# Performance work log

Hardware: AMD Instinct MI355X
Metric: run time of the kernel (lower is better)

## Reference

```python
import jax, jax.numpy as jnp
import numpy as np
import math

B, L, D = 4, 1024, 1024
H, S = 16, 64
HD = D // H
EPS_LN = 1e-12


def _band_logits_init():
    bl = np.zeros((H, S), dtype=np.float32)
    for h in range(H):
        center = (h + 0.5) * (S / max(H, 1.0))
        for s in range(S):
            dist = s + 0.5 - center
            bl[h, s] = -dist * dist
    return jnp.asarray(bl)


def setup_inputs() -> dict:
    key = jax.random.key(0)
    ks = jax.random.split(key, 12)
    std = 1.0 / math.sqrt(D)
    inp = {
        "hidden_states": jax.random.normal(ks[0], (B, L, D), jnp.float32),
        "attention_mask": jnp.zeros((B, 1, 1, L), jnp.float32),
        "cos_phi": jax.random.normal(ks[1], (B, S, L), jnp.float32),
        "sin_phi": jax.random.normal(ks[2], (B, S, L), jnp.float32),
        "mag": jax.random.uniform(ks[3], (B, S, L), jnp.float32),
        "Wq": jax.random.normal(ks[4], (D, D), jnp.float32) * std,
        "bq": jnp.zeros((D,), jnp.float32),
        "Wk": jax.random.normal(ks[5], (D, D), jnp.float32) * std,
        "bk": jnp.zeros((D,), jnp.float32),
        "Wv": jax.random.normal(ks[6], (D, D), jnp.float32) * std,
        "bv": jnp.zeros((D,), jnp.float32),
        "Wo": jax.random.normal(ks[7], (D, D), jnp.float32) * std,
        "bo": jnp.zeros((D,), jnp.float32),
        "band_logits": _band_logits_init(),
        "phase_bias": jnp.full((H,), 0.5, jnp.float32),
        "gamma": jnp.full((H, S), -3.0, jnp.float32),
        "ln_w": jnp.ones((D,), jnp.float32),
        "ln_b": jnp.zeros((D,), jnp.float32),
    }
    return inp


def _shape_heads(x):
    # [B,L,D] -> [B,H,L,HD]
    return x.reshape(B, L, H, HD).transpose(0, 2, 1, 3)


def reference(hidden_states, attention_mask, cos_phi, sin_phi, mag,
              Wq, bq, Wk, bk, Wv, bv, Wo, bo,
              band_logits, phase_bias, gamma, ln_w, ln_b):
    residual = hidden_states
    q = _shape_heads(hidden_states @ Wq.T + bq)
    k = _shape_heads(hidden_states @ Wk.T + bk)
    v = _shape_heads(hidden_states @ Wv.T + bv)

    cos_pl = cos_phi.transpose(0, 2, 1)  # [B,L,S]
    sin_pl = sin_phi.transpose(0, 2, 1)
    mag_pl = mag.transpose(0, 2, 1)
    mag_pl = mag_pl / (mag_pl.mean(axis=-1, keepdims=True) + 1e-8)

    gamma_pos = jax.nn.softplus(gamma)  # [H,S]
    mag_mix = jnp.tanh(jnp.einsum('bls,hs->bhl', mag_pl, gamma_pos))
    scale = 1.0 + 0.5 * mag_mix[..., None]  # [B,H,L,1]
    q = q * scale
    k = k * scale
    v = v * scale

    attn_scores = jnp.einsum('bhld,bhmd->bhlm', q, k) / math.sqrt(HD)

    band_w_sqrt = jnp.sqrt(jax.nn.softmax(band_logits, axis=-1) + 1e-8)  # [H,S]
    cos_feat = cos_pl[:, None] * band_w_sqrt[None, :, None, :]  # [B,H,L,S]
    sin_feat = sin_pl[:, None] * band_w_sqrt[None, :, None, :]
    phase_align = (jnp.einsum('bhls,bhms->bhlm', cos_feat, cos_feat)
                   + jnp.einsum('bhls,bhms->bhlm', sin_feat, sin_feat)) / math.sqrt(S)

    phase_scale = jax.nn.softplus(phase_bias)[None, :, None, None]
    attn_scores = attn_scores + phase_scale * phase_align + attention_mask

    attn_probs = jax.nn.softmax(attn_scores, axis=-1)
    context = jnp.einsum('bhlm,bhmd->bhld', attn_probs, v)
    context = context.transpose(0, 2, 1, 3).reshape(B, L, D)

    out = context @ Wo.T + bo
    x = out + residual
    mu = x.mean(axis=-1, keepdims=True)
    var = ((x - mu) ** 2).mean(axis=-1, keepdims=True)
    return (x - mu) / jnp.sqrt(var + EPS_LN) * ln_w + ln_b
```

## Files before the change

kernel.cpp:

```cpp
#include <hip/hip_runtime.h>
#include <hip/hip_bf16.h>
#include <math.h>

#define DEV __device__ __forceinline__

typedef __attribute__((ext_vector_type(8))) short short8;
typedef __attribute__((ext_vector_type(8))) unsigned short ushort8v;
typedef __attribute__((ext_vector_type(4))) float f32x4;

DEV unsigned short f2bf(float f) {
  unsigned u = __float_as_uint(f);
  u = u + 0x7fffu + ((u >> 16) & 1u);
  return (unsigned short)(u >> 16);
}

DEV float softplus_f(float x) {
  return (x > 20.f) ? x : log1pf(expf(x));
}

DEV int sw64(int r, int e) { return r * 64 + (e ^ (((r) & 7) << 3)); }
DEV int sw128(int r, int e) { return r * 128 + (e ^ (((r) & 7) << 3)); }

#define GL16(gp, lp) __builtin_amdgcn_global_load_lds( \
    (const __attribute__((address_space(1))) unsigned int*)(gp), \
    (__attribute__((address_space(3))) unsigned int*)(lp), 16, 0, 0)

__global__ __launch_bounds__(256) void k_convall(
    const float* __restrict__ hs, const float* __restrict__ wq,
    const float* __restrict__ wk, const float* __restrict__ wv,
    const float* __restrict__ wo, ushort4* __restrict__ hsb4,
    ushort4* __restrict__ wcat4, ushort4* __restrict__ wob4) {
  const int i = blockIdx.x * 256 + threadIdx.x;
  const float* src;
  ushort4* dst;
  int off;
  if (i < 1048576) {
    src = hs; dst = hsb4; off = i;
  } else {
    const int j = i - 1048576;
    const int g = j >> 18;
    off = j & 262143;
    if (g == 0)      { src = wq; dst = wcat4; }
    else if (g == 1) { src = wk; dst = wcat4 + 262144; }
    else if (g == 2) { src = wv; dst = wcat4 + 524288; }
    else             { src = wo; dst = wob4; }
  }
  const float4 v = reinterpret_cast<const float4*>(src)[off];
  ushort4 o;
  o.x = f2bf(v.x); o.y = f2bf(v.y); o.z = f2bf(v.z); o.w = f2bf(v.w);
  dst[off] = o;
}

__global__ __launch_bounds__(256) void k_prep(
    const float* __restrict__ cos_phi, const float* __restrict__ sin_phi,
    const float* __restrict__ mag, const float* __restrict__ band_logits,
    const float* __restrict__ phase_bias, const float* __restrict__ gamma,
    float* __restrict__ scaleB, unsigned short* __restrict__ feat) {
  const int b = blockIdx.x >> 6;
  const int l0 = ((blockIdx.x >> 2) & 15) << 6;
  const int hq = blockIdx.x & 3;
  const int t = threadIdx.x, lane = t & 63, w = t >> 6;
  __shared__ float cosL[64][65];
  __shared__ float sinL[64][65];
  __shared__ float magL[64][65];
  __shared__ float psum[4][64];
  __shared__ float minv[64];
  __shared__ float bwssL[4][64];
  __shared__ float gposL[4][64];

  {
    const int h = (hq << 2) + w;
    float bl = band_logits[h * 64 + lane];
    float mx = bl;
#pragma unroll
    for (int m = 1; m < 64; m <<= 1) mx = fmaxf(mx, __shfl_xor(mx, m));
    float e = __expf(bl - mx);
    float sm = e;
#pragma unroll
    for (int m = 1; m < 64; m <<= 1) sm += __shfl_xor(sm, m);
    const float ps = softplus_f(phase_bias[h]);
    bwssL[w][lane] = sqrtf(e / sm + 1e-8f) * sqrtf(ps * 0.125f);
    gposL[w][lane] = softplus_f(gamma[h * 64 + lane]);
  }

  const size_t boff = (size_t)b * 65536;
  for (int it = 0; it < 16; ++it) {
    const int s = it * 4 + w, l = lane;
    const size_t g = boff + (size_t)s * 1024 + l0 + l;
    cosL[s][l] = cos_phi[g];
    sinL[s][l] = sin_phi[g];
    magL[s][l] = mag[g];
  }
  __syncthreads();
  {
    const int l = t & 63, g = t >> 6;
    float acc = 0.f;
    for (int i = 0; i < 16; ++i) acc += magL[g * 16 + i][l];
    psum[g][l] = acc;
  }
  __syncthreads();
  if (t < 64) {
    float mean = (psum[0][t] + psum[1][t] + psum[2][t] + psum[3][t]) * (1.f / 64.f);
    minv[t] = 1.f / (mean + 1e-8f);
  }
  __syncthreads();
  {
    const int l = lane;
    const float iv = minv[l];
    const int hidx = (hq << 2) + w;
    float acc = 0.f;
    for (int s = 0; s < 64; ++s) acc += magL[s][l] * gposL[w][s];
    const float tnh = tanhf(acc * iv);
    scaleB[(size_t)(((b << 4) + hidx) << 10) + l0 + l] = 1.f + 0.5f * tnh;
  }
  const int l = t >> 2, sq = (t & 3) << 4;
  for (int hh = 0; hh < 4; ++hh) {
    const int h = (hq << 2) + hh;
    unsigned short* fp = feat + ((size_t)(((b << 4) + h) << 10) + l0 + l) * 128;
    unsigned short cb[16], sb[16];
#pragma unroll
    for (int j = 0; j < 16; ++j) {
      const int s = sq + j;
      const float bw = bwssL[hh][s];
      cb[j] = f2bf(bw * cosL[s][l]);
      sb[j] = f2bf(bw * sinL[s][l]);
    }
    *reinterpret_cast<ushort8v*>(fp + sq) = *reinterpret_cast<ushort8v*>(cb);
    *reinterpret_cast<ushort8v*>(fp + sq + 8) = *reinterpret_cast<ushort8v*>(cb + 8);
    *reinterpret_cast<ushort8v*>(fp + 64 + sq) = *reinterpret_cast<ushort8v*>(sb);
    *reinterpret_cast<ushort8v*>(fp + 64 + sq + 8) = *reinterpret_cast<ushort8v*>(sb + 8);
  }
}

template <int MODE>
__global__ __launch_bounds__(256) void k_gemm(
    const unsigned short* __restrict__ A, const unsigned short* __restrict__ Bt,
    int Ntiles, int K,
    const float* __restrict__ bq, const float* __restrict__ bk,
    const float* __restrict__ bv, const float* __restrict__ scaleB,
    unsigned short* __restrict__ qbuf, unsigned short* __restrict__ kbuf,
    unsigned short* __restrict__ vT,
    const float* __restrict__ bo, const float* __restrict__ resid,
    float* __restrict__ xout) {
  __shared__ __align__(16) short As[128 * 64];
  __shared__ __align__(16) short Bs[128 * 64];
  const int t = threadIdx.x;
  const int lane = t & 63;
  const int w = t >> 6;
  const int cpx = gridDim.x >> 3;
  const int swz = (blockIdx.x & 7) * cpx + (blockIdx.x >> 3);
  const int tm = (swz / Ntiles) << 7;
  const int tn = (swz % Ntiles) << 7;
  const int wR = (w >> 1) << 6;
  const int wC = (w & 1) << 6;
  const int rowS = t >> 3;
  const int offS = (t & 7) << 3;
  const int sgm = (rowS & 7) << 3;
  const int ka = (lane >> 4) << 3;
  const int lm = lane & 15;

  const f32x4 vzero = {0.f, 0.f, 0.f, 0.f};
  f32x4 acc[4][4];
#pragma unroll
  for (int i = 0; i < 4; ++i)
#pragma unroll
    for (int j = 0; j < 4; ++j) acc[i][j] = vzero;

  for (int kt = 0; kt < K; kt += 64) {
    __syncthreads();
#pragma unroll
    for (int p = 0; p < 4; ++p) {
      GL16(A + (size_t)(tm + p * 32 + rowS) * K + kt + (offS ^ sgm), (char*)As + p * 4096 + w * 1024);
      GL16(Bt + (size_t)(tn + p * 32 + rowS) * K + kt + (offS ^ sgm), (char*)Bs + p * 4096 + w * 1024);
    }
    __syncthreads();
    short8 af[4][2], bf[4][2];
#pragma unroll
    for (int mt = 0; mt < 4; ++mt) {
      const int r = wR + mt * 16 + lm;
      af[mt][0] = *(const short8*)&As[sw64(r, ka)];
      af[mt][1] = *(const short8*)&As[sw64(r, 32 + ka)];
    }
#pragma unroll
    for (int nt = 0; nt < 4; ++nt) {
      const int r = wC + nt * 16 + lm;
      bf[nt][0] = *(const short8*)&Bs[sw64(r, ka)];
      bf[nt][1] = *(const short8*)&Bs[sw64(r, 32 + ka)];
    }
#pragma unroll
    for (int mt = 0; mt < 4; ++mt)
#pragma unroll
      for (int nt = 0; nt < 4; ++nt) {
        acc[mt][nt] = __builtin_amdgcn_mfma_f32_16x16x32_bf16(af[mt][0], bf[nt][0], acc[mt][nt], 0, 0, 0);
        acc[mt][nt] = __builtin_amdgcn_mfma_f32_16x16x32_bf16(af[mt][1], bf[nt][1], acc[mt][nt], 0, 0, 0);
      }
  }

#pragma unroll
  for (int mt = 0; mt < 4; ++mt) {
#pragma unroll
    for (int r = 0; r < 4; ++r) {
      const int row = tm + wR + mt * 16 + ((lane >> 4) << 2) + r;
#pragma unroll
      for (int nt = 0; nt < 4; ++nt) {
        const int col = tn + wC + nt * 16 + lm;
        float v = acc[mt][nt][r];
        if (MODE == 0) {
          const int b = row >> 10, l = row & 1023;
          const int sect = col >> 10, jj = col & 1023;
          const int h = jj >> 6, hd = jj & 63;
          const int bh = (b << 4) + h;
          const float sc = scaleB[((size_t)bh << 10) + l];
          if (sect == 0) {
            qbuf[((size_t)bh * 1024 + l) * 64 + hd] = f2bf((v + bq[jj]) * sc * 0.125f);
          } else if (sect == 1) {
            kbuf[((size_t)bh * 1024 + l) * 64 + hd] = f2bf((v + bk[jj]) * sc);
          } else {
            vT[(size_t)bh * 65536 + (size_t)hd * 1024 + l] = f2bf((v + bv[jj]) * sc);
          }
        } else {
          xout[(size_t)row * 1024 + col] = v + bo[col] + resid[(size_t)row * 1024 + col];
        }
      }
    }
  }
}

__global__ __launch_bounds__(512) void k_attn(
    const unsigned short* __restrict__ qbuf, const unsigned short* __restrict__ kbuf,
    const unsigned short* __restrict__ vT, const unsigned short* __restrict__ feat,
    const float* __restrict__ maskg, unsigned short* __restrict__ ctx) {
  __shared__ __align__(16) short Kq[64 * 64];
  __shared__ __align__(16) short Kf[64 * 128];
  __shared__ __align__(16) short Vt[64 * 64];
  __shared__ __align__(16) short Pb[8][16 * 64];

  const int t = threadIdx.x, lane = t & 63, w = t >> 6;
  const int bh = blockIdx.x & 63;
  const int qt = blockIdx.x >> 6;
  const int b = bh >> 4, h = bh & 15;
  const int lm = lane & 15;
  const int ka = (lane >> 4) << 3;

  const int rA = t >> 3, oA = (t & 7) << 3;
  const int swA = (rA & 7) << 3;
  const int rF = t >> 4, oF = (t & 15) << 3;
  const int swF = (rF & 7) << 3;
  const int rF2 = rF + 32;
  const int swF2 = (rF2 & 7) << 3;

  const size_t qrow = ((size_t)bh << 10) + qt * 128 + w * 16 + lm;
  short8 aq[2], af[4];
  aq[0] = *(const short8*)(qbuf + qrow * 64 + ka);
  aq[1] = *(const short8*)(qbuf + qrow * 64 + 32 + ka);
#pragma unroll
  for (int kk = 0; kk < 4; ++kk) af[kk] = *(const short8*)(feat + qrow * 128 + kk * 32 + ka);

  short8 ones;
#pragma unroll
  for (int i = 0; i < 8; ++i) ones[i] = (short)0x3F80;

  const f32x4 vzero = {0.f, 0.f, 0.f, 0.f};
  float m_i[4], l_i[4];
  f32x4 o[4];
#pragma unroll
  for (int r = 0; r < 4; ++r) { m_i[r] = -INFINITY; l_i[r] = 0.f; }
#pragma unroll
  for (int nt = 0; nt < 4; ++nt) o[nt] = vzero;

  for (int mt = 0; mt < 16; ++mt) {
    __syncthreads();
    GL16(kbuf + (((size_t)bh << 10) + mt * 64 + rA) * 64 + (oA ^ swA),
         (char*)Kq + w * 1024);
    GL16(vT + ((size_t)bh << 16) + (size_t)rA * 1024 + mt * 64 + (oA ^ swA),
         (char*)Vt + w * 1024);
    GL16(feat + (((size_t)bh << 10) + mt * 64 + rF) * 128 + (oF ^ swF),
         (char*)Kf + w * 1024);
    GL16(feat + (((size_t)bh << 10) + mt * 64 + rF2) * 128 + (oF ^ swF2),
         (char*)Kf + 8192 + w * 1024);
    float mk[4];
#pragma unroll
    for (int nt = 0; nt < 4; ++nt) mk[nt] = maskg[(b << 10) + mt * 64 + nt * 16 + lm];
    __syncthreads();

    f32x4 s[4];
#pragma unroll
    for (int nt = 0; nt < 4; ++nt) s[nt] = vzero;
#pragma unroll
    for (int nt = 0; nt < 4; ++nt) {
      const int rk = nt * 16 + lm;
      s[nt] = __builtin_amdgcn_mfma_f32_16x16x32_bf16(aq[0], *(const short8*)&Kq[sw64(rk, ka)], s[nt], 0, 0, 0);
      s[nt] = __builtin_amdgcn_mfma_f32_16x16x32_bf16(aq[1], *(const short8*)&Kq[sw64(rk, 32 + ka)], s[nt], 0, 0, 0);
#pragma unroll
      for (int kk = 0; kk < 4; ++kk)
        s[nt] = __builtin_amdgcn_mfma_f32_16x16x32_bf16(af[kk], *(const short8*)&Kf[sw128(rk, kk * 32 + ka)], s[nt], 0, 0, 0);
    }

    float pmax[4], al[4];
#pragma unroll
    for (int r = 0; r < 4; ++r) {
      float v0 = fmaxf(fmaxf(s[0][r] + mk[0], s[1][r] + mk[1]),
                       fmaxf(s[2][r] + mk[2], s[3][r] + mk[3]));
#pragma unroll
      for (int m = 1; m < 16; m <<= 1) v0 = fmaxf(v0, __shfl_xor(v0, m));
      pmax[r] = v0;
    }
    int need = 0;
#pragma unroll
    for (int r = 0; r < 4; ++r) need |= (pmax[r] > m_i[r] + 8.f) ? 1 : 0;
    if (__any(need)) {
#pragma unroll
      for (int r = 0; r < 4; ++r) {
        const float mnew = fmaxf(m_i[r], pmax[r]);
        al[r] = __expf(m_i[r] - mnew);
        m_i[r] = mnew;
      }
#pragma unroll
      for (int nt = 0; nt < 4; ++nt)
#pragma unroll
        for (int r = 0; r < 4; ++r) o[nt][r] *= al[r];
    } else {
#pragma unroll
      for (int r = 0; r < 4; ++r) al[r] = 1.f;
    }
#pragma unroll
    for (int nt = 0; nt < 4; ++nt)
#pragma unroll
      for (int r = 0; r < 4; ++r)
        s[nt][r] = __expf(s[nt][r] + mk[nt] - m_i[r]);

    short* Pw = &Pb[w][0];
#pragma unroll
    for (int nt = 0; nt < 4; ++nt)
#pragma unroll
      for (int r = 0; r < 4; ++r) {
        const int prow = ((lane >> 4) << 2) + r;
        Pw[sw64(prow, nt * 16 + lm)] = (short)f2bf(s[nt][r]);
      }

    short8 ap0 = *(const short8*)&Pw[sw64(lm, ka)];
    short8 ap1 = *(const short8*)&Pw[sw64(lm, 32 + ka)];

    f32x4 rs = vzero;
    rs = __builtin_amdgcn_mfma_f32_16x16x32_bf16(ap0, ones, rs, 0, 0, 0);
    rs = __builtin_amdgcn_mfma_f32_16x16x32_bf16(ap1, ones, rs, 0, 0, 0);

#pragma unroll
    for (int nt = 0; nt < 4; ++nt) {
      const int rv = nt * 16 + lm;
      o[nt] = __builtin_amdgcn_mfma_f32_16x16x32_bf16(ap0, *(const short8*)&Vt[sw64(rv, ka)], o[nt], 0, 0, 0);
      o[nt] = __builtin_amdgcn_mfma_f32_16x16x32_bf16(ap1, *(const short8*)&Vt[sw64(rv, 32 + ka)], o[nt], 0, 0, 0);
    }

#pragma unroll
    for (int r = 0; r < 4; ++r) l_i[r] = l_i[r] * al[r] + rs[r];
  }

#pragma unroll
  for (int r = 0; r < 4; ++r) {
    const float inv = 1.f / l_i[r];
    const int row = (b << 10) + qt * 128 + w * 16 + ((lane >> 4) << 2) + r;
#pragma unroll
    for (int nt = 0; nt < 4; ++nt) {
      const int col = (h << 6) + nt * 16 + lm;
      ctx[(size_t)row * 1024 + col] = (short)f2bf(o[nt][r] * inv);
    }
  }
}

__global__ __launch_bounds__(256) void k_ln(const float* __restrict__ x,
                                            const float* __restrict__ lw,
                                            const float* __restrict__ lb,
                                            float* __restrict__ out) {
  const int row = blockIdx.x, t = threadIdx.x, lane = t & 63, w = t >> 6;
  const float4 v = reinterpret_cast<const float4*>(x + (size_t)row * 1024)[t];
  float s = v.x + v.y + v.z + v.w;
  float s2 = v.x * v.x + v.y * v.y + v.z * v.z + v.w * v.w;
#pragma unroll
  for (int m = 1; m < 64; m <<= 1) {
    s += __shfl_xor(s, m);
    s2 += __shfl_xor(s2, m);
  }
  __shared__ float rs[4], rs2[4];
  if (lane == 0) { rs[w] = s; rs2[w] = s2; }
  __syncthreads();
  const float S = rs[0] + rs[1] + rs[2] + rs[3];
  const float S2 = rs2[0] + rs2[1] + rs2[2] + rs2[3];
  const float mu = S * (1.f / 1024.f);
  const float var = fmaxf(S2 * (1.f / 1024.f) - mu * mu, 0.f);
  const float rstd = rsqrtf(var + 1e-12f);
  const float4 wv = reinterpret_cast<const float4*>(lw)[t];
  const float4 bv = reinterpret_cast<const float4*>(lb)[t];
  float4 o;
  o.x = (v.x - mu) * rstd * wv.x + bv.x;
  o.y = (v.y - mu) * rstd * wv.y + bv.y;
  o.z = (v.z - mu) * rstd * wv.z + bv.z;
  o.w = (v.w - mu) * rstd * wv.w + bv.w;
  reinterpret_cast<float4*>(out + (size_t)row * 1024)[t] = o;
}

extern "C" void kernel_launch(void* const* d_in, const int* in_sizes, int n_in,
                              void* d_out, int out_size, void* d_ws, size_t ws_size,
                              hipStream_t stream) {
  const float* hs = (const float*)d_in[0];
  const float* mask = (const float*)d_in[1];
  const float* cosp = (const float*)d_in[2];
  const float* sinp = (const float*)d_in[3];
  const float* mag = (const float*)d_in[4];
  const float* Wq = (const float*)d_in[5];
  const float* bq = (const float*)d_in[6];
  const float* Wk = (const float*)d_in[7];
  const float* bk = (const float*)d_in[8];
  const float* Wv = (const float*)d_in[9];
  const float* bv = (const float*)d_in[10];
  const float* Wo = (const float*)d_in[11];
  const float* bo = (const float*)d_in[12];
  const float* bl = (const float*)d_in[13];
  const float* pb = (const float*)d_in[14];
  const float* gm = (const float*)d_in[15];
  const float* lw = (const float*)d_in[16];
  const float* lbv = (const float*)d_in[17];
  float* outp = (float*)d_out;

  char* ws = (char*)d_ws;
  unsigned short* hsb  = (unsigned short*)(ws);
  unsigned short* wcat = (unsigned short*)(ws + 8388608);
  unsigned short* wob  = (unsigned short*)(ws + 14680064);
  unsigned short* qbuf = (unsigned short*)(ws + 16777216);
  unsigned short* kbuf = (unsigned short*)(ws + 25165824);
  unsigned short* vT   = (unsigned short*)(ws + 33554432);
  unsigned short* feat = (unsigned short*)(ws + 41943040);
  unsigned short* ctx  = (unsigned short*)(ws + 58720256);
  float* scaleB = (float*)(ws + 67108864);
  float* xbuf   = (float*)(ws + 16777216);

  k_convall<<<8192, 256, 0, stream>>>(hs, Wq, Wk, Wv, Wo, (ushort4*)hsb,
                                      (ushort4*)wcat, (ushort4*)wob);
  k_prep<<<256, 256, 0, stream>>>(cosp, sinp, mag, bl, pb, gm, scaleB, feat);
  k_gemm<0><<<32 * 24, 256, 0, stream>>>(hsb, wcat, 24, 1024, bq, bk, bv, scaleB,
                                         qbuf, kbuf, vT, nullptr, nullptr, nullptr);
  k_attn<<<512, 512, 0, stream>>>(qbuf, kbuf, vT, feat, mask, ctx);
  k_gemm<1><<<32 * 8, 256, 0, stream>>>(ctx, wob, 8, 1024, nullptr, nullptr, nullptr,
                                        nullptr, nullptr, nullptr, nullptr, bo, hs, xbuf);
  k_ln<<<4096, 256, 0, stream>>>(xbuf, lw, lbv, outp);
}
```

Baseline: 182.6 us.

## Prefetch next K/V/feature tile into registers during attention compute

Replaces the direct global-to-LDS loads at the top of each attention tile iteration with register staging. The loads for tile mt+1 are issued before the MFMA work on tile mt and written to LDS after it, so global memory latency overlaps with compute. This costs extra VGPRs (four int4 staging registers per thread), which may lower occupancy, and still needs two barriers per iteration.

```diff
diff --git a/kernel.cpp b/kernel.cpp
--- a/kernel.cpp
+++ b/kernel.cpp
@@ -249,6 +249,22 @@
   const int rF2 = rF + 32;
   const int swF2 = (rF2 & 7) << 3;
 
+  int4 stK, stV, stF0, stF1;
+
+#define LOADREGS(mt_) do {                                                                   \
+    stK  = *(const int4*)(kbuf + (((size_t)bh << 10) + (mt_) * 64 + rA) * 64 + (oA ^ swA));  \
+    stV  = *(const int4*)(vT + ((size_t)bh << 16) + (size_t)rA * 1024 + (mt_) * 64 + (oA ^ swA)); \
+    stF0 = *(const int4*)(feat + (((size_t)bh << 10) + (mt_) * 64 + rF) * 128 + (oF ^ swF)); \
+    stF1 = *(const int4*)(feat + (((size_t)bh << 10) + (mt_) * 64 + rF2) * 128 + (oF ^ swF2)); \
+  } while (0)
+
+#define WRITEREGS() do {                                   \
+    *(int4*)((char*)Kq + t * 16) = stK;                    \
+    *(int4*)((char*)Vt + t * 16) = stV;                    \
+    *(int4*)((char*)Kf + t * 16) = stF0;                   \
+    *(int4*)((char*)Kf + 8192 + t * 16) = stF1;            \
+  } while (0)
+
   const size_t qrow = ((size_t)bh << 10) + qt * 128 + w * 16 + lm;
   short8 aq[2], af[4];
   aq[0] = *(const short8*)(qbuf + qrow * 64 + ka);
@@ -268,20 +284,16 @@
 #pragma unroll
   for (int nt = 0; nt < 4; ++nt) o[nt] = vzero;
 
+  LOADREGS(0);
+  WRITEREGS();
+  __syncthreads();
+
   for (int mt = 0; mt < 16; ++mt) {
-    __syncthreads();
-    GL16(kbuf + (((size_t)bh << 10) + mt * 64 + rA) * 64 + (oA ^ swA),
-         (char*)Kq + w * 1024);
-    GL16(vT + ((size_t)bh << 16) + (size_t)rA * 1024 + mt * 64 + (oA ^ swA),
-         (char*)Vt + w * 1024);
-    GL16(feat + (((size_t)bh << 10) + mt * 64 + rF) * 128 + (oF ^ swF),
-         (char*)Kf + w * 1024);
-    GL16(feat + (((size_t)bh << 10) + mt * 64 + rF2) * 128 + (oF ^ swF2),
-         (char*)Kf + 8192 + w * 1024);
+    if (mt < 15) LOADREGS(mt + 1);
+
     float mk[4];
 #pragma unroll
     for (int nt = 0; nt < 4; ++nt) mk[nt] = maskg[(b << 10) + mt * 64 + nt * 16 + lm];
-    __syncthreads();
 
     f32x4 s[4];
 #pragma unroll
@@ -354,7 +366,15 @@
 
 #pragma unroll
     for (int r = 0; r < 4; ++r) l_i[r] = l_i[r] * al[r] + rs[r];
-  }
+
+    __syncthreads();
+    if (mt < 15) {
+      WRITEREGS();
+      __syncthreads();
+    }
+  }
+#undef LOADREGS
+#undef WRITEREGS
 
 #pragma unroll
   for (int r = 0; r < 4; ++r) {
```

New measurement: 182.9 us. Within noise of the previous version (+0.1%).
